# Kernel optimization log

Measured on AMD Instinct MI355X. Metric: run time of the kernel, lower is better.

The kernel has to match this reference:

```python
import jax, jax.numpy as jnp
import numpy as np
from jax import lax

B, LATENT, SEQ, HID, OUT = 4096, 128, 512, 32, 64


def setup_inputs() -> dict:
    key = jax.random.key(0)
    ks = jax.random.split(key, 9)
    s = 1.0 / np.sqrt(HID)  # PyTorch-style init scale
    f32 = jnp.float32
    return {
        "z": jax.random.normal(ks[0], (B, LATENT), f32),
        "init_W": jax.random.uniform(ks[1], (HID, LATENT), f32, -s, s),
        "init_b": jax.random.uniform(ks[2], (HID,), f32, -s, s),
        "W_ih": jax.random.uniform(ks[3], (4 * HID, HID), f32, -s, s),
        "W_hh": jax.random.uniform(ks[4], (4 * HID, HID), f32, -s, s),
        "b_ih": jax.random.uniform(ks[5], (4 * HID,), f32, -s, s),
        "b_hh": jax.random.uniform(ks[6], (4 * HID,), f32, -s, s),
        "out_W": jax.random.uniform(ks[7], (OUT, HID), f32, -s, s),
        "out_b": jax.random.uniform(ks[8], (OUT,), f32, -s, s),
    }


def reference(z, init_W, init_b, W_ih, W_hh, b_ih, b_hh, out_W, out_b):
    # init_fc: z -> h0 (num_layers=1); cell starts at zero
    h0 = z @ init_W.T + init_b  # [B, H]
    c0 = jnp.zeros_like(h0)

    # x_in is all zeros, so the input-to-hidden term is a constant bias;
    # compute it once (keeps W_ih in the graph, matmul with zeros == 0).
    x_zero = jnp.zeros((z.shape[0], W_ih.shape[1]), z.dtype)
    gate_const = x_zero @ W_ih.T + b_ih + b_hh  # [B, 4H]

    def step(carry, _):
        h, c = carry
        gates = h @ W_hh.T + gate_const  # [B, 4H], PyTorch gate order i,f,g,o
        i, f, g, o = jnp.split(gates, 4, axis=-1)
        i = jax.nn.sigmoid(i)
        f = jax.nn.sigmoid(f)
        g = jnp.tanh(g)
        o = jax.nn.sigmoid(o)
        c = f * c + i * g
        h = o * jnp.tanh(c)
        return (h, c), h

    _, hs = lax.scan(step, (h0, c0), None, length=SEQ)  # [T, B, H]
    out = jnp.transpose(hs, (1, 0, 2))  # [B, T, H] (batch_first)
    y = out @ out_W.T + out_b  # [B, T, OUT]
    return y
```

## Files before the change

### kernel.cpp

```cpp
#include <hip/hip_runtime.h>


#define B_SZ   4096
#define LATENT 128
#define SEQ    512
#define HID    32
#define OUT_N  64
#define ROWS   16
#define LSW    40

typedef _Float16 f16x8 __attribute__((ext_vector_type(8)));
typedef _Float16 f16x4 __attribute__((ext_vector_type(4)));
typedef float    f32x4 __attribute__((ext_vector_type(4)));

__device__ __forceinline__ float fexp2(float x) { return __builtin_amdgcn_exp2f(x); }
__device__ __forceinline__ float frcp(float x)  { return __builtin_amdgcn_rcpf(x); }
__device__ __forceinline__ float sigm(float x) {
    return frcp(1.f + fexp2(-1.44269504088896341f * x));
}
__device__ __forceinline__ float tanh_f(float x) {
    return fmaf(-2.f, frcp(1.f + fexp2(2.88539008177792681f * x)), 1.f);
}
__device__ __forceinline__ void lds_barrier() {
    asm volatile("s_waitcnt lgkmcnt(0)\n\ts_barrier" ::: "memory");
}

__global__ __launch_bounds__(512)
void lstm_tr8(const float* __restrict__ z,
              const float* __restrict__ init_W,
              const float* __restrict__ init_b,
              const float* __restrict__ W_hh,
              const float* __restrict__ b_ih,
              const float* __restrict__ b_hh,
              const float* __restrict__ out_W,
              const float* __restrict__ out_b,
              float* __restrict__ y)
{
    __shared__ __align__(16) _Float16 hst[ROWS * LSW];
    __shared__ __align__(8) unsigned short hx[2][2][64][4];

    const int tid  = threadIdx.x;
    const int w    = tid >> 6;
    const int lane = tid & 63;
    const int n_   = lane & 15;
    const int kb   = lane >> 4;
    const int jj   = w & 1;
    const int r_   = w >> 1;
    const int rbase = blockIdx.x * ROWS;

    f16x8 wf[4];
    f32x4 bacc[4];
#pragma unroll
    for (int m = 0; m < 4; m++) {
        int g = 2 * m + jj;
        const float* row = W_hh + (size_t)(16 * g + n_) * HID;
        f16x8 v;
#pragma unroll
        for (int rr = 0; rr < 4; rr++) {
            v[rr]     = (_Float16)row[4 * kb + rr];
            v[4 + rr] = (_Float16)row[4 * kb + 16 + rr];
        }
        wf[m] = v;
        f32x4 b;
#pragma unroll
        for (int r = 0; r < 4; r++) {
            int G = 16 * g + 4 * kb + r;
            b[r] = b_ih[G] + b_hh[G];
        }
        bacc[m] = b;
    }
    f16x8 owf;
    f32x4 oacc;
    {
        int p = r_;
        const float* row = out_W + (size_t)(16 * p + n_) * HID;
        f16x8 v;
#pragma unroll
        for (int rr = 0; rr < 4; rr++) {
            v[rr]     = (_Float16)row[4 * kb + rr];
            v[4 + rr] = (_Float16)row[4 * kb + 16 + rr];
        }
        owf = v;
#pragma unroll
        for (int r = 0; r < 4; r++) oacc[r] = out_b[16 * p + 4 * kb + r];
    }

    {
        int m = tid >> 5, j = tid & 31;
        const float4* zp = (const float4*)(z + (size_t)(rbase + m) * LATENT);
        const float4* wp = (const float4*)(init_W + (size_t)j * LATENT);
        float acc = init_b[j];
#pragma unroll
        for (int k = 0; k < LATENT / 4; k++) {
            float4 a4 = zp[k], b4 = wp[k];
            acc = fmaf(a4.x, b4.x, acc); acc = fmaf(a4.y, b4.y, acc);
            acc = fmaf(a4.z, b4.z, acc); acc = fmaf(a4.w, b4.w, acc);
        }
        hst[m * LSW + j] = (_Float16)acc;
    }
    __syncthreads();

    f16x8 a;
    {
        f16x4 lo = *(const f16x4*)&hst[n_ * LSW + 4 * kb];
        f16x4 hi = *(const f16x4*)&hst[n_ * LSW + 4 * kb + 16];
#pragma unroll
        for (int r = 0; r < 4; r++) { a[r] = lo[r]; a[4 + r] = hi[r]; }
    }

    float c1 = 0.f;

    float* yb = y + (size_t)(rbase + n_) * SEQ * OUT_N + 16 * r_ + 4 * kb;

    for (int t = 0; t < SEQ; t += 4) {
#pragma unroll
        for (int u = 0; u < 4; u++) {
            const int par = u & 1;
            f32x4 acc[4];
#pragma unroll
            for (int m = 0; m < 4; m++)
                acc[m] = __builtin_amdgcn_mfma_f32_16x16x32_f16(wf[m], a, bacc[m], 0, 0, 0);

            {
                float gi = sigm(acc[0][r_]);
                float gf = sigm(acc[1][r_]);
                float gg = tanh_f(acc[2][r_]);
                float go = sigm(acc[3][r_]);
                float cn = fmaf(gf, c1, gi * gg);
                c1 = cn;
                union { _Float16 h; unsigned short u16; } cv;
                cv.h = (_Float16)(go * tanh_f(cn));
                hx[par][jj][lane][r_] = cv.u16;
            }
            lds_barrier();

            f16x4 lo = *(const f16x4*)&hx[par][0][lane][0];
            f16x4 hi = *(const f16x4*)&hx[par][1][lane][0];
#pragma unroll
            for (int r = 0; r < 4; r++) { a[r] = lo[r]; a[4 + r] = hi[r]; }

            if (jj == 0) {
                f32x4 py = __builtin_amdgcn_mfma_f32_16x16x32_f16(owf, a, oacc, 0, 0, 0);
                *(f32x4*)(yb + (size_t)(t + u) * OUT_N) = py;
            }
        }
    }
}

extern "C" void kernel_launch(void* const* d_in, const int* in_sizes, int n_in,
                              void* d_out, int out_size, void* d_ws, size_t ws_size,
                              hipStream_t stream) {
    const float* z      = (const float*)d_in[0];
    const float* init_W = (const float*)d_in[1];
    const float* init_b = (const float*)d_in[2];
    const float* W_hh   = (const float*)d_in[4];
    const float* b_ih   = (const float*)d_in[5];
    const float* b_hh   = (const float*)d_in[6];
    const float* out_W  = (const float*)d_in[7];
    const float* out_b  = (const float*)d_in[8];
    float* yout = (float*)d_out;

    lstm_tr8<<<B_SZ / ROWS, 512, 0, stream>>>(z, init_W, init_b, W_hh, b_ih, b_hh,
                                              out_W, out_b, yout);
}
```

Measured before the change: 633.5 us.

## Permute W_hh rows so one MFMA yields all four gates per lane

```diff
diff --git a/kernel.cpp b/kernel.cpp
--- a/kernel.cpp
+++ b/kernel.cpp
@@ -15,9 +15,6 @@
 
 __device__ __forceinline__ float fexp2(float x) { return __builtin_amdgcn_exp2f(x); }
 __device__ __forceinline__ float frcp(float x)  { return __builtin_amdgcn_rcpf(x); }
-__device__ __forceinline__ float sigm(float x) {
-    return frcp(1.f + fexp2(-1.44269504088896341f * x));
-}
 __device__ __forceinline__ float tanh_f(float x) {
     return fmaf(-2.f, frcp(1.f + fexp2(2.88539008177792681f * x)), 1.f);
 }
@@ -26,18 +23,18 @@
 }
 
 __global__ __launch_bounds__(512)
-void lstm_tr8(const float* __restrict__ z,
-              const float* __restrict__ init_W,
-              const float* __restrict__ init_b,
-              const float* __restrict__ W_hh,
-              const float* __restrict__ b_ih,
-              const float* __restrict__ b_hh,
-              const float* __restrict__ out_W,
-              const float* __restrict__ out_b,
-              float* __restrict__ y)
+void lstm_tr10(const float* __restrict__ z,
+               const float* __restrict__ init_W,
+               const float* __restrict__ init_b,
+               const float* __restrict__ W_hh,
+               const float* __restrict__ b_ih,
+               const float* __restrict__ b_hh,
+               const float* __restrict__ out_W,
+               const float* __restrict__ out_b,
+               float* __restrict__ y)
 {
     __shared__ __align__(16) _Float16 hst[ROWS * LSW];
-    __shared__ __align__(8) unsigned short hx[2][2][64][4];
+    __shared__ __align__(16) unsigned short hx2[2][64][8];
 
     const int tid  = threadIdx.x;
     const int w    = tid >> 6;
@@ -48,39 +45,38 @@
     const int r_   = w >> 1;
     const int rbase = blockIdx.x * ROWS;
 
-    f16x8 wf[4];
-    f32x4 bacc[4];
-#pragma unroll
-    for (int m = 0; m < 4; m++) {
-        int g = 2 * m + jj;
-        const float* row = W_hh + (size_t)(16 * g + n_) * HID;
-        f16x8 v;
+    const float NL2E = -1.44269504088896341f;
+    const float P2L2E = 2.88539008177792681f;
+
+    f16x8 wf1;
+    f32x4 bacc1;
+    {
+        const int arow = 32 * (n_ & 3) + 16 * jj + 4 * (n_ >> 2) + r_;
+        const float asc = ((n_ & 3) == 2) ? P2L2E : NL2E;
+        const float* wrow = W_hh + (size_t)arow * HID;
 #pragma unroll
         for (int rr = 0; rr < 4; rr++) {
-            v[rr]     = (_Float16)row[4 * kb + rr];
-            v[4 + rr] = (_Float16)row[4 * kb + 16 + rr];
+            wf1[rr]     = (_Float16)(asc * wrow[4 * kb + rr]);
+            wf1[4 + rr] = (_Float16)(asc * wrow[16 + 4 * kb + rr]);
         }
-        wf[m] = v;
-        f32x4 b;
 #pragma unroll
         for (int r = 0; r < 4; r++) {
-            int G = 16 * g + 4 * kb + r;
-            b[r] = b_ih[G] + b_hh[G];
+            const int G = 32 * r + 16 * jj + 4 * kb + r_;
+            const float bsc = (r == 2) ? P2L2E : NL2E;
+            bacc1[r] = bsc * (b_ih[G] + b_hh[G]);
         }
-        bacc[m] = b;
     }
+
     f16x8 owf;
     f32x4 oacc;
     {
-        int p = r_;
+        const int p = r_;
         const float* row = out_W + (size_t)(16 * p + n_) * HID;
-        f16x8 v;
 #pragma unroll
         for (int rr = 0; rr < 4; rr++) {
-            v[rr]     = (_Float16)row[4 * kb + rr];
-            v[4 + rr] = (_Float16)row[4 * kb + 16 + rr];
+            owf[rr]     = (_Float16)row[4 * kb + rr];
+            owf[4 + rr] = (_Float16)row[4 * kb + 16 + rr];
         }
-        owf = v;
 #pragma unroll
         for (int r = 0; r < 4; r++) oacc[r] = out_b[16 * p + 4 * kb + r];
     }
@@ -116,30 +112,24 @@
 #pragma unroll
         for (int u = 0; u < 4; u++) {
             const int par = u & 1;
-            f32x4 acc[4];
-#pragma unroll
-            for (int m = 0; m < 4; m++)
-                acc[m] = __builtin_amdgcn_mfma_f32_16x16x32_f16(wf[m], a, bacc[m], 0, 0, 0);
+            f32x4 acc = __builtin_amdgcn_mfma_f32_16x16x32_f16(wf1, a, bacc1, 0, 0, 0);
 
             {
-                float gi = sigm(acc[0][r_]);
-                float gf = sigm(acc[1][r_]);
-                float gg = tanh_f(acc[2][r_]);
-                float go = sigm(acc[3][r_]);
+                float gi = frcp(1.f + fexp2(acc[0]));
+                float gf = frcp(1.f + fexp2(acc[1]));
+                float gg = fmaf(-2.f, frcp(1.f + fexp2(acc[2])), 1.f);
+                float go = frcp(1.f + fexp2(acc[3]));
                 float cn = fmaf(gf, c1, gi * gg);
                 c1 = cn;
                 union { _Float16 h; unsigned short u16; } cv;
                 cv.h = (_Float16)(go * tanh_f(cn));
-                hx[par][jj][lane][r_] = cv.u16;
+                hx2[par][lane][4 * jj + r_] = cv.u16;
             }
             lds_barrier();
 
-            f16x4 lo = *(const f16x4*)&hx[par][0][lane][0];
-            f16x4 hi = *(const f16x4*)&hx[par][1][lane][0];
-#pragma unroll
-            for (int r = 0; r < 4; r++) { a[r] = lo[r]; a[4 + r] = hi[r]; }
+            a = *(const f16x8*)&hx2[par][lane][0];
 
-            if (jj == 0) {
+            if (jj == par) {
                 f32x4 py = __builtin_amdgcn_mfma_f32_16x16x32_f16(owf, a, oacc, 0, 0, 0);
                 *(f32x4*)(yb + (size_t)(t + u) * OUT_N) = py;
             }
@@ -160,6 +150,6 @@
     const float* out_b  = (const float*)d_in[8];
     float* yout = (float*)d_out;
 
-    lstm_tr8<<<B_SZ / ROWS, 512, 0, stream>>>(z, init_W, init_b, W_hh, b_ih, b_hh,
-                                              out_W, out_b, yout);
+    lstm_tr10<<<B_SZ / ROWS, 512, 0, stream>>>(z, init_W, init_b, W_hh, b_ih, b_hh,
+                                               out_W, out_b, yout);
 }
```

After: 605.0 us. -4.5%, faster.
